# Optimization experiments

Hardware: AMD Instinct MI355X
Metric: run time of the kernel (lower is better)

The kernel has to match this reference:

```python
import jax, jax.numpy as jnp
import numpy as np

B, T, F, H = 2048, 512, 64, 20


def setup_inputs() -> dict:
    key = jax.random.key(0)
    ks = jax.random.split(key, 7)
    s = 1.0 / np.sqrt(H)  # PyTorch-style uniform-ish scale, use scaled normal
    return {
        "x": jax.random.normal(ks[0], (B, T, F), dtype=jnp.float32),
        "W_ih": jax.random.normal(ks[1], (4 * H, F), dtype=jnp.float32) * s,
        "W_hh": jax.random.normal(ks[2], (4 * H, H), dtype=jnp.float32) * s,
        "b_ih": jax.random.normal(ks[3], (4 * H,), dtype=jnp.float32) * s,
        "b_hh": jax.random.normal(ks[4], (4 * H,), dtype=jnp.float32) * s,
        "W_lin": jax.random.normal(ks[5], (1, H * T), dtype=jnp.float32) * (1.0 / np.sqrt(H * T)),
        "b_lin": jax.random.normal(ks[6], (1,), dtype=jnp.float32) * 0.01,
    }


def _lstm(x, W_ih, W_hh, b_ih, b_hh):
    # Precompute input contribution for all timesteps: [B,T,4H]
    pre = jnp.einsum("btf,gf->btg", x, W_ih) + b_ih + b_hh
    pre = jnp.transpose(pre, (1, 0, 2))  # [T,B,4H] for scan
    h0 = jnp.zeros((x.shape[0], H), x.dtype)
    c0 = jnp.zeros((x.shape[0], H), x.dtype)

    def step(carry, pre_t):
        h, c = carry
        gates = pre_t + h @ W_hh.T  # [B,4H]
        i_g, f_g, g_g, o_g = jnp.split(gates, 4, axis=-1)  # PyTorch gate order i,f,g,o
        i = jax.nn.sigmoid(i_g)
        f = jax.nn.sigmoid(f_g)
        g = jnp.tanh(g_g)
        o = jax.nn.sigmoid(o_g)
        c_new = f * c + i * g
        h_new = o * jnp.tanh(c_new)
        return (h_new, c_new), h_new

    _, hs = jax.lax.scan(step, (h0, c0), pre)  # hs: [T,B,H]
    return jnp.transpose(hs, (1, 0, 2))  # [B,T,H]


def reference(x, W_ih, W_hh, b_ih, b_hh, W_lin, b_lin):
    lstm_out = _lstm(x, W_ih, W_hh, b_ih, b_hh)          # [B,T,H]
    flat = lstm_out.reshape(x.shape[0], -1)              # [B,T*H]
    return flat @ W_lin.T + b_lin                        # [B,1]
```

## Files before the change

kernel.cpp:

```cpp
#include <hip/hip_runtime.h>

#define NB 2048
#define NT 512
#define NF 64
#define NH 20
#define NG 80
#define TC 8
#define NCHUNK (NT/TC)
#define BPB 3
#define NBLK ((NB + BPB - 1)/BPB)
#define PSTR 85

__device__ __forceinline__ float sigm(float v)   { return 1.0f / (1.0f + __expf(-v)); }
__device__ __forceinline__ float tanh_f(float v) { return 1.0f - 2.0f / (1.0f + __expf(2.0f * v)); }

#define OPAQ4(v) asm volatile("" : "+v"(v.x), "+v"(v.y), "+v"(v.z), "+v"(v.w))

__global__ __launch_bounds__(256, 3) void mv_lstm_fused(
    const float* __restrict__ x, const float* __restrict__ W_ih,
    const float* __restrict__ W_hh, const float* __restrict__ b_ih,
    const float* __restrict__ b_hh, const float* __restrict__ W_lin,
    const float* __restrict__ b_lin, float* __restrict__ out)
{
    __shared__ float w_s[NG][68];
    __shared__ float x_s[2][BPB*TC][68];
    __shared__ float p_s[2][BPB*TC][PSTR];
    __shared__ float bias_s[NG];

    const int tid = threadIdx.x;
    const int b0  = blockIdx.x * BPB;
    const int wtid = tid - 64;

    for (int i = tid; i < NG * 16; i += 256) {
        int r = i >> 4, k4 = i & 15;
        *(float4*)&w_s[r][k4 * 4] = *(const float4*)(W_ih + r * NF + k4 * 4);
    }
    if (tid < NG) bias_s[tid] = b_ih[tid] + b_hh[tid];

    auto stage_x = [&](int cc, int xb) {
        {
            int r = wtid >> 4, k4 = wtid & 15;
            int bb = b0 + (r >> 3);
            int tt = cc * TC + (r & 7);
            float4 v = make_float4(0.f, 0.f, 0.f, 0.f);
            if (bb < NB) v = *(const float4*)(x + ((size_t)bb * NT + tt) * NF + k4 * 4);
            *(float4*)&x_s[xb][r][k4 * 4] = v;
        }
        {
            int id = wtid + 192;
            int r = id >> 4, k4 = id & 15;
            int bb = b0 + (r >> 3);
            int tt = cc * TC + (r & 7);
            float4 v = make_float4(0.f, 0.f, 0.f, 0.f);
            if (bb < NB) v = *(const float4*)(x + ((size_t)bb * NT + tt) * NF + k4 * 4);
            *(float4*)&x_s[xb][r][k4 * 4] = v;
        }
    };

    auto do_gemm = [&](int buf) {
        const int ty = wtid >> 4, tx = wtid & 15;
        float a00=0.f,a01=0.f,a02=0.f,a03=0.f,a04=0.f;
        float a10=0.f,a11=0.f,a12=0.f,a13=0.f,a14=0.f;
        const float* xr0p = &x_s[buf][2*ty+0][0];
        const float* xr1p = &x_s[buf][2*ty+1][0];
        const float* wp0 = &w_s[5*tx+0][0];
        const float* wp1 = &w_s[5*tx+1][0];
        const float* wp2 = &w_s[5*tx+2][0];
        const float* wp3 = &w_s[5*tx+3][0];
        const float* wp4 = &w_s[5*tx+4][0];
        #pragma unroll
        for (int k4 = 0; k4 < 16; ++k4) {
            float4 xv0 = *(const float4*)(xr0p + k4*4);
            float4 xv1 = *(const float4*)(xr1p + k4*4);
            float4 w0  = *(const float4*)(wp0  + k4*4);
            float4 w1  = *(const float4*)(wp1  + k4*4);
            float4 w2  = *(const float4*)(wp2  + k4*4);
            float4 w3  = *(const float4*)(wp3  + k4*4);
            float4 w4  = *(const float4*)(wp4  + k4*4);
            a00=fmaf(xv0.x,w0.x,a00); a00=fmaf(xv0.y,w0.y,a00); a00=fmaf(xv0.z,w0.z,a00); a00=fmaf(xv0.w,w0.w,a00);
            a01=fmaf(xv0.x,w1.x,a01); a01=fmaf(xv0.y,w1.y,a01); a01=fmaf(xv0.z,w1.z,a01); a01=fmaf(xv0.w,w1.w,a01);
            a02=fmaf(xv0.x,w2.x,a02); a02=fmaf(xv0.y,w2.y,a02); a02=fmaf(xv0.z,w2.z,a02); a02=fmaf(xv0.w,w2.w,a02);
            a03=fmaf(xv0.x,w3.x,a03); a03=fmaf(xv0.y,w3.y,a03); a03=fmaf(xv0.z,w3.z,a03); a03=fmaf(xv0.w,w3.w,a03);
            a04=fmaf(xv0.x,w4.x,a04); a04=fmaf(xv0.y,w4.y,a04); a04=fmaf(xv0.z,w4.z,a04); a04=fmaf(xv0.w,w4.w,a04);
            a10=fmaf(xv1.x,w0.x,a10); a10=fmaf(xv1.y,w0.y,a10); a10=fmaf(xv1.z,w0.z,a10); a10=fmaf(xv1.w,w0.w,a10);
            a11=fmaf(xv1.x,w1.x,a11); a11=fmaf(xv1.y,w1.y,a11); a11=fmaf(xv1.z,w1.z,a11); a11=fmaf(xv1.w,w1.w,a11);
            a12=fmaf(xv1.x,w2.x,a12); a12=fmaf(xv1.y,w2.y,a12); a12=fmaf(xv1.z,w2.z,a12); a12=fmaf(xv1.w,w2.w,a12);
            a13=fmaf(xv1.x,w3.x,a13); a13=fmaf(xv1.y,w3.y,a13); a13=fmaf(xv1.z,w3.z,a13); a13=fmaf(xv1.w,w3.w,a13);
            a14=fmaf(xv1.x,w4.x,a14); a14=fmaf(xv1.y,w4.y,a14); a14=fmaf(xv1.z,w4.z,a14); a14=fmaf(xv1.w,w4.w,a14);
        }
        const int r0 = 2*ty, r1 = 2*ty+1, cbase = 5*tx;
        p_s[buf][r0][cbase+0] = a00 + bias_s[cbase+0];
        p_s[buf][r0][cbase+1] = a01 + bias_s[cbase+1];
        p_s[buf][r0][cbase+2] = a02 + bias_s[cbase+2];
        p_s[buf][r0][cbase+3] = a03 + bias_s[cbase+3];
        p_s[buf][r0][cbase+4] = a04 + bias_s[cbase+4];
        p_s[buf][r1][cbase+0] = a10 + bias_s[cbase+0];
        p_s[buf][r1][cbase+1] = a11 + bias_s[cbase+1];
        p_s[buf][r1][cbase+2] = a12 + bias_s[cbase+2];
        p_s[buf][r1][cbase+3] = a13 + bias_s[cbase+3];
        p_s[buf][r1][cbase+4] = a14 + bias_s[cbase+4];
    };

    int bL = tid / NH; if (bL > 2) bL = 2;
    const int j = tid % NH;
    const int base = bL * NH;
    float4 wi0, wi1, wi2, wi3, wi4;
    float4 wf0, wf1, wf2, wf3, wf4;
    float4 wg0, wg1, wg2, wg3, wg4;
    float4 wo0, wo1, wo2, wo3, wo4;
    float ht = 0.f, creg = 0.f, accum = 0.f;

    if (tid < 64) {
        const float* r0 = W_hh + (j)          * NH;
        const float* r1 = W_hh + (NH   + j)   * NH;
        const float* r2 = W_hh + (2*NH + j)   * NH;
        const float* r3 = W_hh + (3*NH + j)   * NH;
        wi0 = *(const float4*)(r0 + 0);  wi1 = *(const float4*)(r0 + 4);
        wi2 = *(const float4*)(r0 + 8);  wi3 = *(const float4*)(r0 + 12);
        wi4 = *(const float4*)(r0 + 16);
        wf0 = *(const float4*)(r1 + 0);  wf1 = *(const float4*)(r1 + 4);
        wf2 = *(const float4*)(r1 + 8);  wf3 = *(const float4*)(r1 + 12);
        wf4 = *(const float4*)(r1 + 16);
        wg0 = *(const float4*)(r2 + 0);  wg1 = *(const float4*)(r2 + 4);
        wg2 = *(const float4*)(r2 + 8);  wg3 = *(const float4*)(r2 + 12);
        wg4 = *(const float4*)(r2 + 16);
        wo0 = *(const float4*)(r3 + 0);  wo1 = *(const float4*)(r3 + 4);
        wo2 = *(const float4*)(r3 + 8);  wo3 = *(const float4*)(r3 + 12);
        wo4 = *(const float4*)(r3 + 16);
        OPAQ4(wi0); OPAQ4(wi1); OPAQ4(wi2); OPAQ4(wi3); OPAQ4(wi4);
        OPAQ4(wf0); OPAQ4(wf1); OPAQ4(wf2); OPAQ4(wf3); OPAQ4(wf4);
        OPAQ4(wg0); OPAQ4(wg1); OPAQ4(wg2); OPAQ4(wg3); OPAQ4(wg4);
        OPAQ4(wo0); OPAQ4(wo1); OPAQ4(wo2); OPAQ4(wo3); OPAQ4(wo4);
    } else {
        stage_x(0, 0);
    }
    __syncthreads();
    if (tid >= 64) {
        do_gemm(0);
        stage_x(1, 1);
    }
    __syncthreads();

#define K4(VWI, VWF, VWG, VWO, KB)                                            \
    {                                                                         \
        float hk0 = __shfl(ht, base + (KB) + 0, 64);                          \
        float hk1 = __shfl(ht, base + (KB) + 1, 64);                          \
        float hk2 = __shfl(ht, base + (KB) + 2, 64);                          \
        float hk3 = __shfl(ht, base + (KB) + 3, 64);                          \
        s0a = fmaf(VWI.x, hk0, s0a); s0b = fmaf(VWI.y, hk1, s0b);             \
        s0a = fmaf(VWI.z, hk2, s0a); s0b = fmaf(VWI.w, hk3, s0b);             \
        s1a = fmaf(VWF.x, hk0, s1a); s1b = fmaf(VWF.y, hk1, s1b);             \
        s1a = fmaf(VWF.z, hk2, s1a); s1b = fmaf(VWF.w, hk3, s1b);             \
        s2a = fmaf(VWG.x, hk0, s2a); s2b = fmaf(VWG.y, hk1, s2b);             \
        s2a = fmaf(VWG.z, hk2, s2a); s2b = fmaf(VWG.w, hk3, s2b);             \
        s3a = fmaf(VWO.x, hk0, s3a); s3b = fmaf(VWO.y, hk1, s3b);             \
        s3a = fmaf(VWO.z, hk2, s3a); s3b = fmaf(VWO.w, hk3, s3b);             \
    }

#define TSTEP(TL, WL)                                                         \
    {                                                                         \
        const float* pr = pc + (TL) * PSTR;                                   \
        float s0a = pr[j],      s0b = 0.f;                                    \
        float s1a = pr[j + 20], s1b = 0.f;                                    \
        float s2a = pr[j + 40], s2b = 0.f;                                    \
        float s3a = pr[j + 60], s3b = 0.f;                                    \
        K4(wi0, wf0, wg0, wo0, 0)  K4(wi1, wf1, wg1, wo1, 4)                  \
        K4(wi2, wf2, wg2, wo2, 8)  K4(wi3, wf3, wg3, wo3, 12)                 \
        K4(wi4, wf4, wg4, wo4, 16)                                            \
        float gi = sigm(s0a + s0b);                                           \
        float gf = sigm(s1a + s1b);                                           \
        float gg = tanh_f(s2a + s2b);                                         \
        float go = sigm(s3a + s3b);                                           \
        creg = gf * creg + gi * gg;                                           \
        ht   = go * tanh_f(creg);                                             \
        accum = fmaf(ht, (WL), accum);                                        \
    }

    for (int c = 0; c < NCHUNK; ++c) {
        if (tid < 64) {
            const int pb = c & 1;
            const float* wlp = W_lin + c * TC * NH + j;
            float wl0 = wlp[0 * NH], wl1 = wlp[1 * NH], wl2 = wlp[2 * NH], wl3 = wlp[3 * NH];
            float wl4 = wlp[4 * NH], wl5 = wlp[5 * NH], wl6 = wlp[6 * NH], wl7 = wlp[7 * NH];
            const float* pc = &p_s[pb][bL * TC][0];
            TSTEP(0, wl0) TSTEP(1, wl1) TSTEP(2, wl2) TSTEP(3, wl3)
            TSTEP(4, wl4) TSTEP(5, wl5) TSTEP(6, wl6) TSTEP(7, wl7)
        } else {
            float4 xr0, xr1;
            const bool doStage = (c + 2 < NCHUNK);
            if (doStage) {
                {
                    int r = wtid >> 4, k4 = wtid & 15;
                    int bb = b0 + (r >> 3);
                    int tt = (c + 2) * TC + (r & 7);
                    xr0 = make_float4(0.f, 0.f, 0.f, 0.f);
                    if (bb < NB) xr0 = *(const float4*)(x + ((size_t)bb * NT + tt) * NF + k4 * 4);
                }
                {
                    int id = wtid + 192;
                    int r = id >> 4, k4 = id & 15;
                    int bb = b0 + (r >> 3);
                    int tt = (c + 2) * TC + (r & 7);
                    xr1 = make_float4(0.f, 0.f, 0.f, 0.f);
                    if (bb < NB) xr1 = *(const float4*)(x + ((size_t)bb * NT + tt) * NF + k4 * 4);
                }
            }
            if (c + 1 < NCHUNK) do_gemm((c + 1) & 1);
            if (doStage) {
                {
                    int r = wtid >> 4, k4 = wtid & 15;
                    *(float4*)&x_s[c & 1][r][k4 * 4] = xr0;
                }
                {
                    int id = wtid + 192;
                    int r = id >> 4, k4 = id & 15;
                    *(float4*)&x_s[c & 1][r][k4 * 4] = xr1;
                }
            }
        }
        __syncthreads();
    }

    if (tid < 64) {
        float tot = 0.f;
        #pragma unroll
        for (int k = 0; k < NH; ++k) tot += __shfl(accum, base + k, 64);
        if (j == 0 && tid < 60 && (b0 + bL) < NB) out[b0 + bL] = tot + b_lin[0];
    }
}

extern "C" void kernel_launch(void* const* d_in, const int* in_sizes, int n_in,
                              void* d_out, int out_size, void* d_ws, size_t ws_size,
                              hipStream_t stream) {
    const float* x     = (const float*)d_in[0];
    const float* W_ih  = (const float*)d_in[1];
    const float* W_hh  = (const float*)d_in[2];
    const float* b_ih  = (const float*)d_in[3];
    const float* b_hh  = (const float*)d_in[4];
    const float* W_lin = (const float*)d_in[5];
    const float* b_lin = (const float*)d_in[6];
    float* outp = (float*)d_out;
    mv_lstm_fused<<<NBLK, 256, 0, stream>>>(x, W_ih, W_hh, b_ih, b_hh, W_lin, b_lin, outp);
}
```

Before: 803.1 us.

## Split block into two recurrence and two GEMM waves with register-staged x

The kernel is restructured so each block handles 4 batch rows with 16-step chunks. Two waves run the recurrence, each covering 2 batch rows, while the other two waves compute the input projection. Those GEMM waves now hold x in registers, read W_ih directly from global memory (scalar-uniform via readfirstlane) instead of shared memory, and drop the x/W shared staging. Biases are folded into the recurrence per lane, and wave roles alternate per block to balance SIMD assignment. This aims to cut shared-memory traffic and synchronization count and to raise recurrence parallelism per CU. The cost is higher register pressure and occupancy lowered to 2 blocks per CU.

```diff
diff --git a/kernel.cpp b/kernel.cpp
--- a/kernel.cpp
+++ b/kernel.cpp
@@ -5,141 +5,16 @@
 #define NF 64
 #define NH 20
 #define NG 80
-#define TC 8
+#define TC 16
 #define NCHUNK (NT/TC)
-#define BPB 3
-#define NBLK ((NB + BPB - 1)/BPB)
+#define BPB 4
+#define NBLK (NB/BPB)
 #define PSTR 85
 
 __device__ __forceinline__ float sigm(float v)   { return 1.0f / (1.0f + __expf(-v)); }
 __device__ __forceinline__ float tanh_f(float v) { return 1.0f - 2.0f / (1.0f + __expf(2.0f * v)); }
 
 #define OPAQ4(v) asm volatile("" : "+v"(v.x), "+v"(v.y), "+v"(v.z), "+v"(v.w))
-
-__global__ __launch_bounds__(256, 3) void mv_lstm_fused(
-    const float* __restrict__ x, const float* __restrict__ W_ih,
-    const float* __restrict__ W_hh, const float* __restrict__ b_ih,
-    const float* __restrict__ b_hh, const float* __restrict__ W_lin,
-    const float* __restrict__ b_lin, float* __restrict__ out)
-{
-    __shared__ float w_s[NG][68];
-    __shared__ float x_s[2][BPB*TC][68];
-    __shared__ float p_s[2][BPB*TC][PSTR];
-    __shared__ float bias_s[NG];
-
-    const int tid = threadIdx.x;
-    const int b0  = blockIdx.x * BPB;
-    const int wtid = tid - 64;
-
-    for (int i = tid; i < NG * 16; i += 256) {
-        int r = i >> 4, k4 = i & 15;
-        *(float4*)&w_s[r][k4 * 4] = *(const float4*)(W_ih + r * NF + k4 * 4);
-    }
-    if (tid < NG) bias_s[tid] = b_ih[tid] + b_hh[tid];
-
-    auto stage_x = [&](int cc, int xb) {
-        {
-            int r = wtid >> 4, k4 = wtid & 15;
-            int bb = b0 + (r >> 3);
-            int tt = cc * TC + (r & 7);
-            float4 v = make_float4(0.f, 0.f, 0.f, 0.f);
-            if (bb < NB) v = *(const float4*)(x + ((size_t)bb * NT + tt) * NF + k4 * 4);
-            *(float4*)&x_s[xb][r][k4 * 4] = v;
-        }
-        {
-            int id = wtid + 192;
-            int r = id >> 4, k4 = id & 15;
-            int bb = b0 + (r >> 3);
-            int tt = cc * TC + (r & 7);
-            float4 v = make_float4(0.f, 0.f, 0.f, 0.f);
-            if (bb < NB) v = *(const float4*)(x + ((size_t)bb * NT + tt) * NF + k4 * 4);
-            *(float4*)&x_s[xb][r][k4 * 4] = v;
-        }
-    };
-
-    auto do_gemm = [&](int buf) {
-        const int ty = wtid >> 4, tx = wtid & 15;
-        float a00=0.f,a01=0.f,a02=0.f,a03=0.f,a04=0.f;
-        float a10=0.f,a11=0.f,a12=0.f,a13=0.f,a14=0.f;
-        const float* xr0p = &x_s[buf][2*ty+0][0];
-        const float* xr1p = &x_s[buf][2*ty+1][0];
-        const float* wp0 = &w_s[5*tx+0][0];
-        const float* wp1 = &w_s[5*tx+1][0];
-        const float* wp2 = &w_s[5*tx+2][0];
-        const float* wp3 = &w_s[5*tx+3][0];
-        const float* wp4 = &w_s[5*tx+4][0];
-        #pragma unroll
-        for (int k4 = 0; k4 < 16; ++k4) {
-            float4 xv0 = *(const float4*)(xr0p + k4*4);
-            float4 xv1 = *(const float4*)(xr1p + k4*4);
-            float4 w0  = *(const float4*)(wp0  + k4*4);
-            float4 w1  = *(const float4*)(wp1  + k4*4);
-            float4 w2  = *(const float4*)(wp2  + k4*4);
-            float4 w3  = *(const float4*)(wp3  + k4*4);
-            float4 w4  = *(const float4*)(wp4  + k4*4);
-            a00=fmaf(xv0.x,w0.x,a00); a00=fmaf(xv0.y,w0.y,a00); a00=fmaf(xv0.z,w0.z,a00); a00=fmaf(xv0.w,w0.w,a00);
-            a01=fmaf(xv0.x,w1.x,a01); a01=fmaf(xv0.y,w1.y,a01); a01=fmaf(xv0.z,w1.z,a01); a01=fmaf(xv0.w,w1.w,a01);
-            a02=fmaf(xv0.x,w2.x,a02); a02=fmaf(xv0.y,w2.y,a02); a02=fmaf(xv0.z,w2.z,a02); a02=fmaf(xv0.w,w2.w,a02);
-            a03=fmaf(xv0.x,w3.x,a03); a03=fmaf(xv0.y,w3.y,a03); a03=fmaf(xv0.z,w3.z,a03); a03=fmaf(xv0.w,w3.w,a03);
-            a04=fmaf(xv0.x,w4.x,a04); a04=fmaf(xv0.y,w4.y,a04); a04=fmaf(xv0.z,w4.z,a04); a04=fmaf(xv0.w,w4.w,a04);
-            a10=fmaf(xv1.x,w0.x,a10); a10=fmaf(xv1.y,w0.y,a10); a10=fmaf(xv1.z,w0.z,a10); a10=fmaf(xv1.w,w0.w,a10);
-            a11=fmaf(xv1.x,w1.x,a11); a11=fmaf(xv1.y,w1.y,a11); a11=fmaf(xv1.z,w1.z,a11); a11=fmaf(xv1.w,w1.w,a11);
-            a12=fmaf(xv1.x,w2.x,a12); a12=fmaf(xv1.y,w2.y,a12); a12=fmaf(xv1.z,w2.z,a12); a12=fmaf(xv1.w,w2.w,a12);
-            a13=fmaf(xv1.x,w3.x,a13); a13=fmaf(xv1.y,w3.y,a13); a13=fmaf(xv1.z,w3.z,a13); a13=fmaf(xv1.w,w3.w,a13);
-            a14=fmaf(xv1.x,w4.x,a14); a14=fmaf(xv1.y,w4.y,a14); a14=fmaf(xv1.z,w4.z,a14); a14=fmaf(xv1.w,w4.w,a14);
-        }
-        const int r0 = 2*ty, r1 = 2*ty+1, cbase = 5*tx;
-        p_s[buf][r0][cbase+0] = a00 + bias_s[cbase+0];
-        p_s[buf][r0][cbase+1] = a01 + bias_s[cbase+1];
-        p_s[buf][r0][cbase+2] = a02 + bias_s[cbase+2];
-        p_s[buf][r0][cbase+3] = a03 + bias_s[cbase+3];
-        p_s[buf][r0][cbase+4] = a04 + bias_s[cbase+4];
-        p_s[buf][r1][cbase+0] = a10 + bias_s[cbase+0];
-        p_s[buf][r1][cbase+1] = a11 + bias_s[cbase+1];
-        p_s[buf][r1][cbase+2] = a12 + bias_s[cbase+2];
-        p_s[buf][r1][cbase+3] = a13 + bias_s[cbase+3];
-        p_s[buf][r1][cbase+4] = a14 + bias_s[cbase+4];
-    };
-
-    int bL = tid / NH; if (bL > 2) bL = 2;
-    const int j = tid % NH;
-    const int base = bL * NH;
-    float4 wi0, wi1, wi2, wi3, wi4;
-    float4 wf0, wf1, wf2, wf3, wf4;
-    float4 wg0, wg1, wg2, wg3, wg4;
-    float4 wo0, wo1, wo2, wo3, wo4;
-    float ht = 0.f, creg = 0.f, accum = 0.f;
-
-    if (tid < 64) {
-        const float* r0 = W_hh + (j)          * NH;
-        const float* r1 = W_hh + (NH   + j)   * NH;
-        const float* r2 = W_hh + (2*NH + j)   * NH;
-        const float* r3 = W_hh + (3*NH + j)   * NH;
-        wi0 = *(const float4*)(r0 + 0);  wi1 = *(const float4*)(r0 + 4);
-        wi2 = *(const float4*)(r0 + 8);  wi3 = *(const float4*)(r0 + 12);
-        wi4 = *(const float4*)(r0 + 16);
-        wf0 = *(const float4*)(r1 + 0);  wf1 = *(const float4*)(r1 + 4);
-        wf2 = *(const float4*)(r1 + 8);  wf3 = *(const float4*)(r1 + 12);
-        wf4 = *(const float4*)(r1 + 16);
-        wg0 = *(const float4*)(r2 + 0);  wg1 = *(const float4*)(r2 + 4);
-        wg2 = *(const float4*)(r2 + 8);  wg3 = *(const float4*)(r2 + 12);
-        wg4 = *(const float4*)(r2 + 16);
-        wo0 = *(const float4*)(r3 + 0);  wo1 = *(const float4*)(r3 + 4);
-        wo2 = *(const float4*)(r3 + 8);  wo3 = *(const float4*)(r3 + 12);
-        wo4 = *(const float4*)(r3 + 16);
-        OPAQ4(wi0); OPAQ4(wi1); OPAQ4(wi2); OPAQ4(wi3); OPAQ4(wi4);
-        OPAQ4(wf0); OPAQ4(wf1); OPAQ4(wf2); OPAQ4(wf3); OPAQ4(wf4);
-        OPAQ4(wg0); OPAQ4(wg1); OPAQ4(wg2); OPAQ4(wg3); OPAQ4(wg4);
-        OPAQ4(wo0); OPAQ4(wo1); OPAQ4(wo2); OPAQ4(wo3); OPAQ4(wo4);
-    } else {
-        stage_x(0, 0);
-    }
-    __syncthreads();
-    if (tid >= 64) {
-        do_gemm(0);
-        stage_x(1, 1);
-    }
-    __syncthreads();
 
 #define K4(VWI, VWF, VWG, VWO, KB)                                            \
     {                                                                         \
@@ -157,13 +32,13 @@
         s3a = fmaf(VWO.z, hk2, s3a); s3b = fmaf(VWO.w, hk3, s3b);             \
     }
 
-#define TSTEP(TL, WL)                                                         \
+#define TSTEP(TL)                                                             \
     {                                                                         \
         const float* pr = pc + (TL) * PSTR;                                   \
-        float s0a = pr[j],      s0b = 0.f;                                    \
-        float s1a = pr[j + 20], s1b = 0.f;                                    \
-        float s2a = pr[j + 40], s2b = 0.f;                                    \
-        float s3a = pr[j + 60], s3b = 0.f;                                    \
+        float s0a = pr[j]      + bias_i, s0b = 0.f;                           \
+        float s1a = pr[j + 20] + bias_f, s1b = 0.f;                           \
+        float s2a = pr[j + 40] + bias_g, s2b = 0.f;                           \
+        float s3a = pr[j + 60] + bias_o, s3b = 0.f;                           \
         K4(wi0, wf0, wg0, wo0, 0)  K4(wi1, wf1, wg1, wo1, 4)                  \
         K4(wi2, wf2, wg2, wo2, 8)  K4(wi3, wf3, wg3, wo3, 12)                 \
         K4(wi4, wf4, wg4, wo4, 16)                                            \
@@ -173,59 +48,126 @@
         float go = sigm(s3a + s3b);                                           \
         creg = gf * creg + gi * gg;                                           \
         ht   = go * tanh_f(creg);                                             \
-        accum = fmaf(ht, (WL), accum);                                        \
+        accum = fmaf(ht, wlp[(TL) * NH], accum);                              \
     }
 
+#define GFMA(AV, WV) { AV = fmaf(xv.x, WV.x, AV); AV = fmaf(xv.y, WV.y, AV);  \
+                       AV = fmaf(xv.z, WV.z, AV); AV = fmaf(xv.w, WV.w, AV); }
+
+__global__ __launch_bounds__(256, 2) void mv_lstm_fused(
+    const float* __restrict__ x, const float* __restrict__ W_ih,
+    const float* __restrict__ W_hh, const float* __restrict__ b_ih,
+    const float* __restrict__ b_hh, const float* __restrict__ W_lin,
+    const float* __restrict__ b_lin, float* __restrict__ out)
+{
+    __shared__ float p_s[2][BPB*TC][PSTR];
+
+    const int tid  = threadIdx.x;
+    const int lane = tid & 63;
+    const int wv   = tid >> 6;
+    const int b0   = blockIdx.x * BPB;
+
+    const int  swapr = (int)(blockIdx.x & 1u);
+    const bool isRec = swapr ? (wv >= 2) : (wv < 2);
+    const int  rw    = swapr ? (wv - 2) : wv;
+    const int  gw    = swapr ? wv       : (wv - 2);
+
+    const int j = lane % NH;
+    int wbL = lane / NH; if (wbL > 1) wbL = 1;
+    const int base = wbL * NH;
+
+    float4 wi0,wi1,wi2,wi3,wi4, wf0,wf1,wf2,wf3,wf4,
+           wg0,wg1,wg2,wg3,wg4, wo0,wo1,wo2,wo3,wo4;
+    float bias_i=0.f, bias_f=0.f, bias_g=0.f, bias_o=0.f;
+    float ht=0.f, creg=0.f, accum=0.f;
+
+    float4 xr[16];
+    const float* wbase = W_ih;
+    const float* xrow  = x;
+
+    auto gbody = [&](int m) {
+        float* prow = &p_s[m & 1][lane][0] + (gw * 40);
+        #pragma unroll 1
+        for (int g = 0; g < 8; ++g) {
+            const float* wr = wbase + (size_t)(5 * g) * NF;
+            float a0=0.f, a1=0.f, a2=0.f, a3=0.f, a4=0.f;
+            #pragma unroll
+            for (int k4 = 0; k4 < 16; ++k4) {
+                const float4 xv = xr[k4];
+                const float4 w0 = *(const float4*)(wr + 0*NF + 4*k4);
+                const float4 w1 = *(const float4*)(wr + 1*NF + 4*k4);
+                const float4 w2 = *(const float4*)(wr + 2*NF + 4*k4);
+                const float4 w3 = *(const float4*)(wr + 3*NF + 4*k4);
+                const float4 w4 = *(const float4*)(wr + 4*NF + 4*k4);
+                GFMA(a0, w0) GFMA(a1, w1) GFMA(a2, w2) GFMA(a3, w3) GFMA(a4, w4)
+            }
+            prow[5*g+0] = a0; prow[5*g+1] = a1; prow[5*g+2] = a2;
+            prow[5*g+3] = a3; prow[5*g+4] = a4;
+        }
+        if (m + 1 < NCHUNK) {
+            const float* xp = xrow + (size_t)(m + 1) * TC * NF;
+            #pragma unroll
+            for (int k4 = 0; k4 < 16; ++k4)
+                xr[k4] = *(const float4*)(xp + 4*k4);
+        }
+    };
+
+    if (isRec) {
+        const float* r0 = W_hh + (size_t)(j)        * NH;
+        const float* r1 = W_hh + (size_t)(NH   + j) * NH;
+        const float* r2 = W_hh + (size_t)(2*NH + j) * NH;
+        const float* r3 = W_hh + (size_t)(3*NH + j) * NH;
+        wi0 = *(const float4*)(r0 + 0);  wi1 = *(const float4*)(r0 + 4);
+        wi2 = *(const float4*)(r0 + 8);  wi3 = *(const float4*)(r0 + 12);
+        wi4 = *(const float4*)(r0 + 16);
+        wf0 = *(const float4*)(r1 + 0);  wf1 = *(const float4*)(r1 + 4);
+        wf2 = *(const float4*)(r1 + 8);  wf3 = *(const float4*)(r1 + 12);
+        wf4 = *(const float4*)(r1 + 16);
+        wg0 = *(const float4*)(r2 + 0);  wg1 = *(const float4*)(r2 + 4);
+        wg2 = *(const float4*)(r2 + 8);  wg3 = *(const float4*)(r2 + 12);
+        wg4 = *(const float4*)(r2 + 16);
+        wo0 = *(const float4*)(r3 + 0);  wo1 = *(const float4*)(r3 + 4);
+        wo2 = *(const float4*)(r3 + 8);  wo3 = *(const float4*)(r3 + 12);
+        wo4 = *(const float4*)(r3 + 16);
+        OPAQ4(wi0); OPAQ4(wi1); OPAQ4(wi2); OPAQ4(wi3); OPAQ4(wi4);
+        OPAQ4(wf0); OPAQ4(wf1); OPAQ4(wf2); OPAQ4(wf3); OPAQ4(wf4);
+        OPAQ4(wg0); OPAQ4(wg1); OPAQ4(wg2); OPAQ4(wg3); OPAQ4(wg4);
+        OPAQ4(wo0); OPAQ4(wo1); OPAQ4(wo2); OPAQ4(wo3); OPAQ4(wo4);
+        bias_i = b_ih[j]        + b_hh[j];
+        bias_f = b_ih[NH + j]   + b_hh[NH + j];
+        bias_g = b_ih[2*NH + j] + b_hh[2*NH + j];
+        bias_o = b_ih[3*NH + j] + b_hh[3*NH + j];
+    } else {
+        const int c0 = __builtin_amdgcn_readfirstlane(gw * 40);
+        wbase = W_ih + (size_t)c0 * NF;
+        xrow  = x + ((size_t)(b0 + (lane >> 4)) * NT + (lane & 15)) * NF;
+        #pragma unroll
+        for (int k4 = 0; k4 < 16; ++k4)
+            xr[k4] = *(const float4*)(xrow + 4*k4);
+        gbody(0);
+    }
+    __syncthreads();
+
     for (int c = 0; c < NCHUNK; ++c) {
-        if (tid < 64) {
-            const int pb = c & 1;
+        if (isRec) {
+            const float* pc  = &p_s[c & 1][(rw * 2 + wbL) * TC][0];
             const float* wlp = W_lin + c * TC * NH + j;
-            float wl0 = wlp[0 * NH], wl1 = wlp[1 * NH], wl2 = wlp[2 * NH], wl3 = wlp[3 * NH];
-            float wl4 = wlp[4 * NH], wl5 = wlp[5 * NH], wl6 = wlp[6 * NH], wl7 = wlp[7 * NH];
-            const float* pc = &p_s[pb][bL * TC][0];
-            TSTEP(0, wl0) TSTEP(1, wl1) TSTEP(2, wl2) TSTEP(3, wl3)
-            TSTEP(4, wl4) TSTEP(5, wl5) TSTEP(6, wl6) TSTEP(7, wl7)
+            TSTEP(0)  TSTEP(1)  TSTEP(2)  TSTEP(3)
+            TSTEP(4)  TSTEP(5)  TSTEP(6)  TSTEP(7)
+            TSTEP(8)  TSTEP(9)  TSTEP(10) TSTEP(11)
+            TSTEP(12) TSTEP(13) TSTEP(14) TSTEP(15)
         } else {
-            float4 xr0, xr1;
-            const bool doStage = (c + 2 < NCHUNK);
-            if (doStage) {
-                {
-                    int r = wtid >> 4, k4 = wtid & 15;
-                    int bb = b0 + (r >> 3);
-                    int tt = (c + 2) * TC + (r & 7);
-                    xr0 = make_float4(0.f, 0.f, 0.f, 0.f);
-                    if (bb < NB) xr0 = *(const float4*)(x + ((size_t)bb * NT + tt) * NF + k4 * 4);
-                }
-                {
-                    int id = wtid + 192;
-                    int r = id >> 4, k4 = id & 15;
-                    int bb = b0 + (r >> 3);
-                    int tt = (c + 2) * TC + (r & 7);
-                    xr1 = make_float4(0.f, 0.f, 0.f, 0.f);
-                    if (bb < NB) xr1 = *(const float4*)(x + ((size_t)bb * NT + tt) * NF + k4 * 4);
-                }
-            }
-            if (c + 1 < NCHUNK) do_gemm((c + 1) & 1);
-            if (doStage) {
-                {
-                    int r = wtid >> 4, k4 = wtid & 15;
-                    *(float4*)&x_s[c & 1][r][k4 * 4] = xr0;
-                }
-                {
-                    int id = wtid + 192;
-                    int r = id >> 4, k4 = id & 15;
-                    *(float4*)&x_s[c & 1][r][k4 * 4] = xr1;
-                }
-            }
+            if (c + 1 < NCHUNK) gbody(c + 1);
         }
         __syncthreads();
     }
 
-    if (tid < 64) {
+    if (isRec) {
         float tot = 0.f;
         #pragma unroll
         for (int k = 0; k < NH; ++k) tot += __shfl(accum, base + k, 64);
-        if (j == 0 && tid < 60 && (b0 + bL) < NB) out[b0 + bL] = tot + b_lin[0];
+        if (j == 0 && lane < 2 * NH)
+            out[b0 + rw * 2 + wbL] = tot + b_lin[0];
     }
 }
 
```

After: 1.998 ms. +148.8%, slower.
